# Optimization experiments

Measured on AMD Instinct MI355X. Metric: run time of the kernel, lower is better.

Reference implementation:

```python
import jax, jax.numpy as jnp
import numpy as np

N = 25000      # nodes
E = 400000     # edges
IN = 1024      # in_channels
FC = 128       # feature_channels
ADD = 20       # additional_channels
MID = (FC + ADD) // 4   # 37, fc1 output (heads=4)
OUT = 3
EPS = 1e-5
NEG_SLOPE = 0.01


def setup_inputs() -> dict:
    key = jax.random.key(0)
    ks = jax.random.split(key, 16)
    d = {}
    d["features"] = jax.random.normal(ks[0], (N, IN), dtype=jnp.float32)
    d["edges"] = jax.random.randint(ks[1], (2, E), 0, N, dtype=jnp.int64)
    d["edges2"] = jax.random.randint(ks[2], (2, 1000), 0, N, dtype=jnp.int64)
    d["edge_features"] = jax.random.normal(ks[3], (E, 1), dtype=jnp.float32)
    d["additional_feature"] = jax.random.normal(ks[4], (N, ADD), dtype=jnp.float32)
    # SAGEConv params: lin_l (neighbor path, with bias), lin_r (root path, no bias)
    s = 1.0 / np.sqrt(IN)
    d["Wl"] = jax.random.uniform(ks[5], (FC, IN), jnp.float32, -s, s)
    d["bl"] = jax.random.uniform(ks[6], (FC,), jnp.float32, -s, s)
    d["Wr"] = jax.random.uniform(ks[7], (FC, IN), jnp.float32, -s, s)
    s1 = 1.0 / np.sqrt(FC + ADD)
    d["W1"] = jax.random.uniform(ks[8], (MID, FC + ADD), jnp.float32, -s1, s1)
    d["b1"] = jax.random.uniform(ks[9], (MID,), jnp.float32, -s1, s1)
    s2 = 1.0 / np.sqrt(MID)
    d["W2"] = jax.random.uniform(ks[10], (OUT, MID), jnp.float32, -s2, s2)
    d["b2"] = jax.random.uniform(ks[11], (OUT,), jnp.float32, -s2, s2)
    # BatchNorm1d (eval mode -> running stats)
    d["gamma"] = jnp.ones((MID,), jnp.float32)
    d["beta"] = jnp.zeros((MID,), jnp.float32)
    d["run_mean"] = jax.random.normal(ks[12], (MID,), dtype=jnp.float32) * 0.1
    d["run_var"] = jnp.abs(jax.random.normal(ks[13], (MID,), dtype=jnp.float32)) * 0.1 + 1.0
    return d


def reference(features, edges, edges2, edge_features, additional_feature,
              Wl, bl, Wr, W1, b1, W2, b2, gamma, beta, run_mean, run_var):
    src, dst = edges[0], edges[1]  # PyG: messages flow source -> target
    # scatter-mean of neighbor features onto targets
    agg = jax.ops.segment_sum(features[src], dst, num_segments=N)        # [N, IN]
    deg = jax.ops.segment_sum(jnp.ones((E,), features.dtype), dst, num_segments=N)
    agg = agg / jnp.maximum(deg, 1.0)[:, None]
    # SAGEConv: lin_l(mean_neigh) + lin_r(x)
    x = agg @ Wl.T + bl + features @ Wr.T                                 # [N, FC]
    x = jnp.where(x >= 0, x, NEG_SLOPE * x)                               # leaky_relu
    # dropout is identity in eval mode
    x = jnp.concatenate([x, additional_feature], axis=1) @ W1.T + b1      # [N, MID]
    x = jnp.maximum(x, 0.0)                                               # relu
    x = gamma * (x - run_mean) * jax.lax.rsqrt(run_var + EPS) + beta      # BN eval
    return x @ W2.T + b2                                                  # [N, OUT]
```

## Files before the change

### kernel.cpp

```cpp
#include <hip/hip_runtime.h>

#define N_NODES 25000
#define N_EDGES 400000
#define IN_CH 1024
#define FC 128
#define ADD_CH 20
#define XCH 148
#define MID 37
#define OUT_CH 3
#define MAXDEG 64

typedef short bf16x8 __attribute__((ext_vector_type(8)));
typedef float f32x4 __attribute__((ext_vector_type(4)));

__device__ __forceinline__ unsigned int f2bf(float x) {
    unsigned int u = __builtin_bit_cast(unsigned int, x);
    unsigned int lsb = (u >> 16) & 1u;
    u += 0x7fffu + lsb;
    return u >> 16;
}
__device__ __forceinline__ unsigned int pkbf(float a, float b) {
    return f2bf(a) | (f2bf(b) << 16);
}
__device__ __forceinline__ float bflo(unsigned int v) {
    return __builtin_bit_cast(float, v << 16);
}
__device__ __forceinline__ float bfhi(unsigned int v) {
    return __builtin_bit_cast(float, v & 0xffff0000u);
}

#define WSWZ_B 16
#define BUILD_B 1563

__global__ __launch_bounds__(256) void prep_kernel(const float* __restrict__ Wl,
                                                   const float* __restrict__ Wr,
                                                   const int* __restrict__ edges,
                                                   ushort* __restrict__ Wpk,
                                                   int* __restrict__ cursor,
                                                   int* __restrict__ col) {
    int b = blockIdx.x, t = threadIdx.x;
    if (b < WSWZ_B) {
        int w = t >> 6, lane = t & 63, l15 = lane & 15, q8 = (lane >> 4) * 8;
        int ch = b * 16 + l15;
        const float* src = (ch < FC) ? (Wl + (size_t)ch * IN_CH)
                                     : (Wr + (size_t)(ch - FC) * IN_CH);
        #pragma unroll
        for (int j = 0; j < 8; ++j) {
            int kt = w * 8 + j;
            float4 lo = *(const float4*)(src + kt * 32 + q8);
            float4 hi = *(const float4*)(src + kt * 32 + q8 + 4);
            uint4 pk;
            pk.x = pkbf(lo.x, lo.y); pk.y = pkbf(lo.z, lo.w);
            pk.z = pkbf(hi.x, hi.y); pk.w = pkbf(hi.z, hi.w);
            ((uint4*)Wpk)[(size_t)(b * 32 + kt) * 64 + lane] = pk;
        }
    } else {
        int e = (b - WSWZ_B) * 256 + t;
        if (e < N_EDGES) {
            int dst = edges[N_EDGES + e];
            int pos = atomicAdd(&cursor[dst], 1);
            if (pos < MAXDEG) col[dst * MAXDEG + pos] = edges[e];
        }
    }
}

__global__ __launch_bounds__(256, 2) void gemm_kernel(const float* __restrict__ A,
                                                      const ushort* __restrict__ Wpk,
                                                      ushort* __restrict__ Py,
                                                      ushort* __restrict__ Pz) {
    __shared__ __align__(16) ushort Fs[2 * 32 * 64 * 8];
    int t = threadIdx.x, w = t >> 6, lane = t & 63;
    int l15 = lane & 15, q = lane >> 4;
    int m0 = blockIdx.x * 32;

    const bf16x8* Wf = (const bf16x8*)Wpk + (size_t)(w * 4) * 32 * 64 + lane;

    {
        int r = t >> 3;
        int p0 = t & 7;
        int row = m0 + r; if (row >= N_NODES) row = N_NODES - 1;
        const float* src = A + (size_t)row * IN_CH;
        int g = r >> 4, l = r & 15;
        #pragma unroll
        for (int h = 0; h < 2; ++h) {
            float4 lo[8], hi[8];
            #pragma unroll
            for (int m = 0; m < 8; ++m) {
                int o = (h * 8 + m) * 8 + p0;
                lo[m] = *(const float4*)(src + o * 8);
                hi[m] = *(const float4*)(src + o * 8 + 4);
            }
            #pragma unroll
            for (int m = 0; m < 8; ++m) {
                int o = (h * 8 + m) * 8 + p0;
                int kt = o >> 2, qq = o & 3;
                uint4 pk;
                pk.x = pkbf(lo[m].x, lo[m].y); pk.y = pkbf(lo[m].z, lo[m].w);
                pk.z = pkbf(hi[m].x, hi[m].y); pk.w = pkbf(hi[m].z, hi[m].w);
                int u = (g * 32 + kt) * 64 + qq * 16 + ((l + qq) & 15);
                *(uint4*)&Fs[(size_t)u * 8] = pk;
            }
        }
    }
    __syncthreads();

    int ru = q * 16 + ((l15 + q) & 15);
    const bf16x8* F0 = (const bf16x8*)Fs + (0 * 32) * 64 + ru;
    const bf16x8* F1 = (const bf16x8*)Fs + (1 * 32) * 64 + ru;

    f32x4 acc[4][2] = {};
    bf16x8 aw[2][4], an[2][4], bw[2][2], bn[2][2];
    #pragma unroll
    for (int cf = 0; cf < 4; ++cf) {
        aw[0][cf] = Wf[(size_t)(cf * 32 + 0) * 64];
        aw[1][cf] = Wf[(size_t)(cf * 32 + 1) * 64];
    }
    bw[0][0] = F0[0 * 64]; bw[0][1] = F1[0 * 64];
    bw[1][0] = F0[1 * 64]; bw[1][1] = F1[1 * 64];

    for (int kt = 0; kt < 32; kt += 2) {
        int kn = kt + 2;
        if (kn < 32) {
            #pragma unroll
            for (int cf = 0; cf < 4; ++cf) {
                an[0][cf] = Wf[(size_t)(cf * 32 + kn) * 64];
                an[1][cf] = Wf[(size_t)(cf * 32 + kn + 1) * 64];
            }
            bn[0][0] = F0[(size_t)kn * 64];       bn[0][1] = F1[(size_t)kn * 64];
            bn[1][0] = F0[(size_t)(kn + 1) * 64]; bn[1][1] = F1[(size_t)(kn + 1) * 64];
        }
        #pragma unroll
        for (int j = 0; j < 2; ++j)
            #pragma unroll
            for (int cf = 0; cf < 4; ++cf) {
                acc[cf][0] = __builtin_amdgcn_mfma_f32_16x16x32_bf16(aw[j][cf], bw[j][0], acc[cf][0], 0, 0, 0);
                acc[cf][1] = __builtin_amdgcn_mfma_f32_16x16x32_bf16(aw[j][cf], bw[j][1], acc[cf][1], 0, 0, 0);
            }
        #pragma unroll
        for (int j = 0; j < 2; ++j) {
            #pragma unroll
            for (int cf = 0; cf < 4; ++cf) aw[j][cf] = an[j][cf];
            bw[j][0] = bn[j][0]; bw[j][1] = bn[j][1];
        }
    }
    #pragma unroll
    for (int g = 0; g < 2; ++g) {
        int node = m0 + g * 16 + l15;
        if (node < N_NODES) {
            ushort* base = (w < 2) ? (Py + (size_t)node * FC + w * 64)
                                   : (Pz + (size_t)node * FC + (w - 2) * 64);
            #pragma unroll
            for (int cf = 0; cf < 4; ++cf) {
                f32x4 v = acc[cf][g];
                uint2 pk;
                pk.x = pkbf(v[0], v[1]);
                pk.y = pkbf(v[2], v[3]);
                *(uint2*)(base + cf * 16 + q * 4) = pk;
            }
        }
    }
}

__global__ __launch_bounds__(256) void fused_tail(const ushort* __restrict__ Py,
                                                  const ushort* __restrict__ Pz,
                                                  const int* __restrict__ deg,
                                                  const int* __restrict__ col,
                                                  const float* __restrict__ addf,
                                                  const float* __restrict__ bl,
                                                  const float* __restrict__ W1,
                                                  const float* __restrict__ b1,
                                                  const float* __restrict__ W2,
                                                  const float* __restrict__ b2,
                                                  const float* __restrict__ gamma,
                                                  const float* __restrict__ beta,
                                                  const float* __restrict__ rmean,
                                                  const float* __restrict__ rvar,
                                                  float* __restrict__ out) {
    __shared__ float W1s[XCH][MID + 3];
    __shared__ float xbuf[4][XCH + 4];
    __shared__ float hbuf[4][MID + 3];
    int t = threadIdx.x;
    for (int idx = t; idx < MID * XCH; idx += 256) {
        int j = idx / XCH, k = idx - j * XCH;
        W1s[k][j] = W1[idx];
    }
    __syncthreads();
    int w = t >> 6, lane = t & 63;
    int n = blockIdx.x * 4 + w;
    bool valid = (n < N_NODES);
    int d = valid ? deg[n] : 0;
    if (d > MAXDEG) d = MAXDEG;
    int g = lane >> 4, c16 = lane & 15;
    float s[8] = {0.f, 0.f, 0.f, 0.f, 0.f, 0.f, 0.f, 0.f};
    if (d > 0) {
        int cidx = col[n * MAXDEG + (lane < d ? lane : 0)];
        for (int i = 0; i < d; i += 16) {
            int e[4];
            uint4 v[4];
            #pragma unroll
            for (int j = 0; j < 4; ++j) {
                int ee = i + g + j * 4;
                e[j] = __shfl(cidx, (ee < d) ? ee : 0);
            }
            #pragma unroll
            for (int j = 0; j < 4; ++j)
                v[j] = *(const uint4*)&Py[(size_t)e[j] * FC + c16 * 8];
            #pragma unroll
            for (int j = 0; j < 4; ++j) {
                if (i + g + j * 4 < d) {
                    s[0] += bflo(v[j].x); s[1] += bfhi(v[j].x);
                    s[2] += bflo(v[j].y); s[3] += bfhi(v[j].y);
                    s[4] += bflo(v[j].z); s[5] += bfhi(v[j].z);
                    s[6] += bflo(v[j].w); s[7] += bfhi(v[j].w);
                }
            }
        }
        #pragma unroll
        for (int r = 0; r < 8; ++r) {
            s[r] += __shfl_xor(s[r], 16);
            s[r] += __shfl_xor(s[r], 32);
        }
    }
    if (valid) {
        if (lane < 16) {
            #pragma unroll
            for (int r = 0; r < 8; ++r) xbuf[w][lane * 8 + r] = s[r];
        }
        float invd = 1.0f / (float)(d > 1 ? d : 1);
        unsigned int vr = *(const unsigned int*)&Pz[(size_t)n * FC + lane * 2];
        float x0 = xbuf[w][2 * lane] * invd + bl[2 * lane] + bflo(vr);
        float x1 = xbuf[w][2 * lane + 1] * invd + bl[2 * lane + 1] + bfhi(vr);
        x0 = (x0 >= 0.f) ? x0 : 0.01f * x0;
        x1 = (x1 >= 0.f) ? x1 : 0.01f * x1;
        xbuf[w][2 * lane] = x0;
        xbuf[w][2 * lane + 1] = x1;
        if (lane < ADD_CH) xbuf[w][FC + lane] = addf[(size_t)n * ADD_CH + lane];
        if (lane < MID) {
            float h = b1[lane];
            #pragma unroll 4
            for (int k = 0; k < XCH; ++k) h += W1s[k][lane] * xbuf[w][k];
            h = fmaxf(h, 0.0f);
            h = gamma[lane] * (h - rmean[lane]) * rsqrtf(rvar[lane] + 1e-5f) + beta[lane];
            hbuf[w][lane] = h;
        }
        if (lane < OUT_CH) {
            float o = b2[lane];
            #pragma unroll
            for (int j = 0; j < MID; ++j) o += W2[lane * MID + j] * hbuf[w][j];
            out[(size_t)n * OUT_CH + lane] = o;
        }
    }
}


extern "C" void kernel_launch(void* const* d_in, const int* in_sizes, int n_in,
                              void* d_out, int out_size, void* d_ws, size_t ws_size,
                              hipStream_t stream) {
    const float* features = (const float*)d_in[0];
    const int*   edges    = (const int*)d_in[1];
    const float* addf     = (const float*)d_in[4];
    const float* Wl       = (const float*)d_in[5];
    const float* bl       = (const float*)d_in[6];
    const float* Wr       = (const float*)d_in[7];
    const float* W1       = (const float*)d_in[8];
    const float* b1       = (const float*)d_in[9];
    const float* W2       = (const float*)d_in[10];
    const float* b2       = (const float*)d_in[11];
    const float* gamma    = (const float*)d_in[12];
    const float* beta     = (const float*)d_in[13];
    const float* rmean    = (const float*)d_in[14];
    const float* rvar     = (const float*)d_in[15];
    float* out = (float*)d_out;

    char* ws = (char*)d_ws;
    size_t off = 0;
    ushort* Py = (ushort*)(ws + off);     off += (size_t)N_NODES * FC * 2;
    ushort* Pz = (ushort*)(ws + off);     off += (size_t)N_NODES * FC * 2;
    ushort* Wpk = (ushort*)(ws + off);    off += (size_t)16 * 32 * 64 * 16;
    int* cursor = (int*)(ws + off);       off += (size_t)N_NODES * 4;
    int* col = (int*)(ws + off);          off += (size_t)N_NODES * MAXDEG * 4;

    (void)hipMemsetAsync(cursor, 0, (size_t)N_NODES * 4, stream);

    prep_kernel<<<WSWZ_B + BUILD_B, 256, 0, stream>>>(Wl, Wr, edges, Wpk, cursor, col);

    gemm_kernel<<<(N_NODES + 31) / 32, 256, 0, stream>>>(features, Wpk, Py, Pz);

    fused_tail<<<(N_NODES + 3) / 4, 256, 0, stream>>>(Py, Pz, cursor, col, addf, bl,
                                                      W1, b1, W2, b2, gamma, beta,
                                                      rmean, rvar, out);
}
```

Measured before the change: 295.1 us.

## Fuse edge-bucket build into GEMM launch and widen GEMM blocks to 512 threads

The separate memset of the degree cursor moves into the prep kernel, which now only zeroes cursors and packs weights. The edge bucketing (atomic cursor plus column fill) runs as extra blocks of the GEMM launch, so it overlaps with the MFMA work instead of serialising before it. The GEMM block grows to 8 waves with 2 output fragments per wave instead of 4, which lowers register pressure and raises occupancy. The cost is that each wave reloads the shared feature tile for fewer outputs, and atomic-heavy build blocks now compete with GEMM blocks for compute units.

```diff
diff --git a/kernel.cpp b/kernel.cpp
--- a/kernel.cpp
+++ b/kernel.cpp
@@ -30,14 +30,12 @@
 }
 
 #define WSWZ_B 16
-#define BUILD_B 1563
+#define ZERO_B 98
 
 __global__ __launch_bounds__(256) void prep_kernel(const float* __restrict__ Wl,
                                                    const float* __restrict__ Wr,
-                                                   const int* __restrict__ edges,
                                                    ushort* __restrict__ Wpk,
-                                                   int* __restrict__ cursor,
-                                                   int* __restrict__ col) {
+                                                   int* __restrict__ cursor) {
     int b = blockIdx.x, t = threadIdx.x;
     if (b < WSWZ_B) {
         int w = t >> 6, lane = t & 63, l15 = lane & 15, q8 = (lane >> 4) * 8;
@@ -55,44 +53,54 @@
             ((uint4*)Wpk)[(size_t)(b * 32 + kt) * 64 + lane] = pk;
         }
     } else {
-        int e = (b - WSWZ_B) * 256 + t;
+        int i = (b - WSWZ_B) * 256 + t;
+        if (i < N_NODES) cursor[i] = 0;
+    }
+}
+
+#define GEMM_B 782
+#define BUILD_B 782
+
+__global__ __launch_bounds__(512, 4) void gemm_build(const float* __restrict__ A,
+                                                     const ushort* __restrict__ Wpk,
+                                                     ushort* __restrict__ Py,
+                                                     ushort* __restrict__ Pz,
+                                                     const int* __restrict__ edges,
+                                                     int* __restrict__ cursor,
+                                                     int* __restrict__ col) {
+    __shared__ __align__(16) ushort Fs[2 * 32 * 64 * 8];
+    int b = blockIdx.x, t = threadIdx.x;
+    if (b >= GEMM_B) {
+        int e = (b - GEMM_B) * 512 + t;
         if (e < N_EDGES) {
             int dst = edges[N_EDGES + e];
             int pos = atomicAdd(&cursor[dst], 1);
             if (pos < MAXDEG) col[dst * MAXDEG + pos] = edges[e];
         }
-    }
-}
-
-__global__ __launch_bounds__(256, 2) void gemm_kernel(const float* __restrict__ A,
-                                                      const ushort* __restrict__ Wpk,
-                                                      ushort* __restrict__ Py,
-                                                      ushort* __restrict__ Pz) {
-    __shared__ __align__(16) ushort Fs[2 * 32 * 64 * 8];
-    int t = threadIdx.x, w = t >> 6, lane = t & 63;
+        return;
+    }
+    int w = t >> 6, lane = t & 63;
     int l15 = lane & 15, q = lane >> 4;
-    int m0 = blockIdx.x * 32;
-
-    const bf16x8* Wf = (const bf16x8*)Wpk + (size_t)(w * 4) * 32 * 64 + lane;
+    int m0 = b * 32;
 
     {
-        int r = t >> 3;
-        int p0 = t & 7;
+        int r = t >> 4;
+        int p0 = t & 15;
         int row = m0 + r; if (row >= N_NODES) row = N_NODES - 1;
         const float* src = A + (size_t)row * IN_CH;
         int g = r >> 4, l = r & 15;
         #pragma unroll
         for (int h = 0; h < 2; ++h) {
-            float4 lo[8], hi[8];
-            #pragma unroll
-            for (int m = 0; m < 8; ++m) {
-                int o = (h * 8 + m) * 8 + p0;
+            float4 lo[4], hi[4];
+            #pragma unroll
+            for (int m = 0; m < 4; ++m) {
+                int o = (h * 4 + m) * 16 + p0;
                 lo[m] = *(const float4*)(src + o * 8);
                 hi[m] = *(const float4*)(src + o * 8 + 4);
             }
             #pragma unroll
-            for (int m = 0; m < 8; ++m) {
-                int o = (h * 8 + m) * 8 + p0;
+            for (int m = 0; m < 4; ++m) {
+                int o = (h * 4 + m) * 16 + p0;
                 int kt = o >> 2, qq = o & 3;
                 uint4 pk;
                 pk.x = pkbf(lo[m].x, lo[m].y); pk.y = pkbf(lo[m].z, lo[m].w);
@@ -105,52 +113,49 @@
     __syncthreads();
 
     int ru = q * 16 + ((l15 + q) & 15);
-    const bf16x8* F0 = (const bf16x8*)Fs + (0 * 32) * 64 + ru;
-    const bf16x8* F1 = (const bf16x8*)Fs + (1 * 32) * 64 + ru;
-
-    f32x4 acc[4][2] = {};
-    bf16x8 aw[2][4], an[2][4], bw[2][2], bn[2][2];
-    #pragma unroll
-    for (int cf = 0; cf < 4; ++cf) {
-        aw[0][cf] = Wf[(size_t)(cf * 32 + 0) * 64];
-        aw[1][cf] = Wf[(size_t)(cf * 32 + 1) * 64];
-    }
-    bw[0][0] = F0[0 * 64]; bw[0][1] = F1[0 * 64];
-    bw[1][0] = F0[1 * 64]; bw[1][1] = F1[1 * 64];
+    const bf16x8* F0 = (const bf16x8*)Fs + ru;
+    const bf16x8* F1 = (const bf16x8*)Fs + 32 * 64 + ru;
+    const bf16x8* W0 = (const bf16x8*)Wpk + (size_t)(w * 2 + 0) * 32 * 64 + lane;
+    const bf16x8* W1 = (const bf16x8*)Wpk + (size_t)(w * 2 + 1) * 32 * 64 + lane;
+
+    f32x4 acc[2][2] = {};
+    bf16x8 aw[2][2], an[2][2], bw[2][2], bn[2][2];
+    aw[0][0] = W0[0];  aw[0][1] = W1[0];
+    aw[1][0] = W0[64]; aw[1][1] = W1[64];
+    bw[0][0] = F0[0];  bw[0][1] = F1[0];
+    bw[1][0] = F0[64]; bw[1][1] = F1[64];
 
     for (int kt = 0; kt < 32; kt += 2) {
         int kn = kt + 2;
         if (kn < 32) {
-            #pragma unroll
-            for (int cf = 0; cf < 4; ++cf) {
-                an[0][cf] = Wf[(size_t)(cf * 32 + kn) * 64];
-                an[1][cf] = Wf[(size_t)(cf * 32 + kn + 1) * 64];
-            }
+            an[0][0] = W0[(size_t)kn * 64];       an[0][1] = W1[(size_t)kn * 64];
+            an[1][0] = W0[(size_t)(kn + 1) * 64]; an[1][1] = W1[(size_t)(kn + 1) * 64];
             bn[0][0] = F0[(size_t)kn * 64];       bn[0][1] = F1[(size_t)kn * 64];
             bn[1][0] = F0[(size_t)(kn + 1) * 64]; bn[1][1] = F1[(size_t)(kn + 1) * 64];
         }
         #pragma unroll
         for (int j = 0; j < 2; ++j)
             #pragma unroll
-            for (int cf = 0; cf < 4; ++cf) {
+            for (int cf = 0; cf < 2; ++cf) {
                 acc[cf][0] = __builtin_amdgcn_mfma_f32_16x16x32_bf16(aw[j][cf], bw[j][0], acc[cf][0], 0, 0, 0);
                 acc[cf][1] = __builtin_amdgcn_mfma_f32_16x16x32_bf16(aw[j][cf], bw[j][1], acc[cf][1], 0, 0, 0);
             }
         #pragma unroll
-        for (int j = 0; j < 2; ++j) {
-            #pragma unroll
-            for (int cf = 0; cf < 4; ++cf) aw[j][cf] = an[j][cf];
-            bw[j][0] = bn[j][0]; bw[j][1] = bn[j][1];
-        }
+        for (int j = 0; j < 2; ++j)
+            #pragma unroll
+            for (int cf = 0; cf < 2; ++cf) {
+                aw[j][cf] = an[j][cf];
+                bw[j][cf] = bn[j][cf];
+            }
     }
     #pragma unroll
     for (int g = 0; g < 2; ++g) {
         int node = m0 + g * 16 + l15;
         if (node < N_NODES) {
-            ushort* base = (w < 2) ? (Py + (size_t)node * FC + w * 64)
-                                   : (Pz + (size_t)node * FC + (w - 2) * 64);
-            #pragma unroll
-            for (int cf = 0; cf < 4; ++cf) {
+            ushort* base = (w < 4) ? (Py + (size_t)node * FC + w * 32)
+                                   : (Pz + (size_t)node * FC + (w - 4) * 32);
+            #pragma unroll
+            for (int cf = 0; cf < 2; ++cf) {
                 f32x4 v = acc[cf][g];
                 uint2 pk;
                 pk.x = pkbf(v[0], v[1]);
@@ -280,11 +285,10 @@
     int* cursor = (int*)(ws + off);       off += (size_t)N_NODES * 4;
     int* col = (int*)(ws + off);          off += (size_t)N_NODES * MAXDEG * 4;
 
-    (void)hipMemsetAsync(cursor, 0, (size_t)N_NODES * 4, stream);
-
-    prep_kernel<<<WSWZ_B + BUILD_B, 256, 0, stream>>>(Wl, Wr, edges, Wpk, cursor, col);
-
-    gemm_kernel<<<(N_NODES + 31) / 32, 256, 0, stream>>>(features, Wpk, Py, Pz);
+    prep_kernel<<<WSWZ_B + ZERO_B, 256, 0, stream>>>(Wl, Wr, Wpk, cursor);
+
+    gemm_build<<<GEMM_B + BUILD_B, 512, 0, stream>>>(features, Wpk, Py, Pz,
+                                                     edges, cursor, col);
 
     fused_tail<<<(N_NODES + 3) / 4, 256, 0, stream>>>(Py, Pz, cursor, col, addf, bl,
                                                       W1, b1, W2, b2, gamma, beta,
```

After: 270.9 us. 8.2% less time.
